# Kernel optimization log

Hardware: AMD Instinct MI355X
Metric: run time of the kernel (lower is better)

## Reference

```python
import jax, jax.numpy as jnp
import numpy as np

EMBED_DIM = 1024


def setup_inputs() -> dict:
    key = jax.random.key(0)
    ks = jax.random.split(key, 9)
    B, S, D = 4, 4096, EMBED_DIM
    s = 1.0 / np.sqrt(D)
    inp = {"x": jax.random.normal(ks[0], (B, S, D), dtype=jnp.float32)}
    names = ["q", "k", "v", "out"]
    for i, n in enumerate(names):
        inp[f"w_{n}"] = jax.random.uniform(ks[1 + 2 * i], (D, D), jnp.float32, -s, s)
        inp[f"b_{n}"] = jax.random.uniform(ks[2 + 2 * i], (D,), jnp.float32, -s, s)
    return inp


def reference(x, w_q, b_q, w_k, b_k, w_v, b_v, w_out, b_out):
    D = x.shape[-1]
    scaling = 1.0 / jnp.sqrt(jnp.asarray(D, x.dtype))
    q = jnp.einsum("bsd,ed->bse", x, w_q) + b_q
    k = jnp.einsum("bsd,ed->bse", x, w_k) + b_k
    v = jnp.einsum("bsd,ed->bse", x, w_v) + b_v
    # full [B, S, S] attention matrix, as in the original module
    scores = jnp.einsum("bqd,bkd->bqk", q, k) * scaling
    attn = jax.nn.softmax(scores, axis=-1)
    out = jnp.einsum("bqk,bkd->bqd", attn, v)
    return jnp.einsum("bsd,ed->bse", out, w_out) + b_out
```

## Files before the change

### kernel.cpp

```cpp
#include <hip/hip_runtime.h>
#include <hip/hip_bf16.h>

typedef __hip_bfloat16 bf16;
typedef __bf16 bf16x8 __attribute__((ext_vector_type(8)));
typedef float f32x4 __attribute__((ext_vector_type(4)));

#define B_ 4
#define S_ 4096
#define D_ 1024
#define BS_ 16384
#define N3_ 3072

__device__ __forceinline__ void gld_lds16(const void* g, void* l) {
    __builtin_amdgcn_global_load_lds(
        (const __attribute__((address_space(1))) void*)g,
        (__attribute__((address_space(3))) void*)l, 16, 0, 0);
}

__device__ __forceinline__ void cast4_one(const float* __restrict__ in,
                                          bf16* __restrict__ out, int i) {
    float4 v = ((const float4*)in)[i];
    union { ushort4 u; bf16 h[4]; } cv;
    cv.h[0] = __float2bfloat16(v.x);
    cv.h[1] = __float2bfloat16(v.y);
    cv.h[2] = __float2bfloat16(v.z);
    cv.h[3] = __float2bfloat16(v.w);
    ((ushort4*)out)[i] = cv.u;
}

__global__ __launch_bounds__(256) void prologue(
    const float* __restrict__ x, const float* __restrict__ wq,
    const float* __restrict__ wk, const float* __restrict__ wv,
    const float* __restrict__ wo, const float* __restrict__ bq,
    const float* __restrict__ bk, const float* __restrict__ bv,
    bf16* __restrict__ xb, bf16* __restrict__ Wc, bf16* __restrict__ Wo,
    float* __restrict__ bc, float* __restrict__ ls) {
    const int blk = blockIdx.x, tid = threadIdx.x;
    if (blk < 16384) {
        cast4_one(x, xb, blk * 256 + tid);
    } else if (blk < 20480) {
        int w = (blk - 16384) >> 10;
        int i = ((blk - 16384) & 1023) * 256 + tid;
        const float* src = (w == 0) ? wq : (w == 1) ? wk : (w == 2) ? wv : wo;
        bf16* dst = (w == 3) ? Wo : Wc + (long)w * D_ * D_;
        cast4_one(src, dst, i);
    } else if (blk < 20544) {
        ls[(blk - 20480) * 256 + tid] = 0.f;
    } else {
        for (int i = tid; i < N3_; i += 256)
            bc[i] = (i < 1024) ? bq[i] : (i < 2048) ? bk[i - 1024] : bv[i - 2048];
    }
}

__global__ __launch_bounds__(256) void transpose_v(const bf16* __restrict__ QKV,
                                                   bf16* __restrict__ VT) {
    __shared__ bf16 t[32][33];
    const int b = blockIdx.z;
    const bf16* Vb = QKV + (long)b * S_ * N3_ + 2048;
    bf16* VTb = VT + (long)b * D_ * S_;
    const int s0 = blockIdx.x * 32, d0 = blockIdx.y * 32;
    const int r = threadIdx.x >> 5, c = threadIdx.x & 31;
#pragma unroll
    for (int i = 0; i < 4; i++)
        t[r + i * 8][c] = Vb[(long)(s0 + r + i * 8) * N3_ + d0 + c];
    __syncthreads();
#pragma unroll
    for (int i = 0; i < 4; i++)
        VTb[(long)(d0 + r + i * 8) * S_ + s0 + c] = t[c][r + i * 8];
}

template <int EPI, int BM>
__global__ __launch_bounds__(256, 2) void gemm_nt(
    const bf16* __restrict__ A, int lda, long sA,
    const bf16* __restrict__ B, int ldb, long sB,
    void* __restrict__ Cout, int ldc, long sC,
    int K, const float* __restrict__ bias,
    float* __restrict__ rowsum, int sL, float scale) {
    constexpr int MI = BM / 32;
    __shared__ __align__(16) bf16 As[BM * 64];
    __shared__ __align__(16) bf16 Bs[128 * 64];
    const int tid = threadIdx.x;
    const int lane = tid & 63;
    const int wave = tid >> 6;
    const int bz = blockIdx.z;
    const int m0 = blockIdx.x * BM, n0 = blockIdx.y * 128;
    A += (long)bz * sA;
    B += (long)bz * sB;
    rowsum += (long)bz * sL;

    const int wr = (wave >> 1) * (BM / 2);
    const int wc = (wave & 1) * 64;
    const int fm = lane & 15;
    const int q4 = lane >> 4;
    const int sw = fm & 7;
    const int rd0 = ((q4 ^ sw) << 3);
    const int rd1 = (((4 + q4) ^ sw) << 3);

    f32x4 zero = {0.f, 0.f, 0.f, 0.f};
    f32x4 acc[MI][4];
#pragma unroll
    for (int i = 0; i < MI; i++)
#pragma unroll
        for (int j = 0; j < 4; j++) acc[i][j] = zero;

    for (int k0 = 0; k0 < K; k0 += 64) {
#pragma unroll
        for (int t = 0; t < BM / 32; t++) {
            int c = tid + t * 256;
            int row = c >> 3;
            int q = (((c & 7) ^ (row & 7)) << 3);
            gld_lds16(A + (long)(m0 + row) * lda + k0 + q, As + c * 8);
        }
#pragma unroll
        for (int t = 0; t < 4; t++) {
            int c = tid + t * 256;
            int row = c >> 3;
            int q = (((c & 7) ^ (row & 7)) << 3);
            gld_lds16(B + (long)(n0 + row) * ldb + k0 + q, Bs + c * 8);
        }
        __syncthreads();
#pragma unroll
        for (int kh = 0; kh < 2; kh++) {
            const int rdo = kh ? rd1 : rd0;
            bf16x8 af[MI], bfr[4];
#pragma unroll
            for (int i = 0; i < MI; i++)
                af[i] = *(const bf16x8*)(As + (wr + i * 16 + fm) * 64 + rdo);
#pragma unroll
            for (int j = 0; j < 4; j++)
                bfr[j] = *(const bf16x8*)(Bs + (wc + j * 16 + fm) * 64 + rdo);
#pragma unroll
            for (int i = 0; i < MI; i++)
#pragma unroll
                for (int j = 0; j < 4; j++)
                    acc[i][j] = __builtin_amdgcn_mfma_f32_16x16x32_bf16(
                        af[i], bfr[j], acc[i][j], 0, 0, 0);
        }
        __syncthreads();
    }

#pragma unroll
    for (int i = 0; i < MI; i++)
#pragma unroll
        for (int r = 0; r < 4; r++) {
            const int grow = m0 + wr + q4 * 4 + i * 16 + r;
            if constexpr (EPI == 0) {
#pragma unroll
                for (int j = 0; j < 4; j++) {
                    int gcol = n0 + wc + j * 16 + fm;
                    ((bf16*)Cout)[(long)bz * sC + (long)grow * ldc + gcol] =
                        __float2bfloat16(acc[i][j][r] + bias[gcol]);
                }
            } else if constexpr (EPI == 1) {
                float s = 0.f;
#pragma unroll
                for (int j = 0; j < 4; j++) {
                    int gcol = n0 + wc + j * 16 + fm;
                    float v = __expf(acc[i][j][r] * scale);
                    bf16 hv = __float2bfloat16(v);
                    ((bf16*)Cout)[(long)bz * sC + (long)grow * ldc + gcol] = hv;
                    s += __bfloat162float(hv);
                }
                s += __shfl_xor(s, 1, 16);
                s += __shfl_xor(s, 2, 16);
                s += __shfl_xor(s, 4, 16);
                s += __shfl_xor(s, 8, 16);
                if (fm == 0) atomicAdd(rowsum + grow, s);
            } else if constexpr (EPI == 2) {
                float inv = 1.0f / rowsum[grow];
#pragma unroll
                for (int j = 0; j < 4; j++) {
                    int gcol = n0 + wc + j * 16 + fm;
                    ((bf16*)Cout)[(long)bz * sC + (long)grow * ldc + gcol] =
                        __float2bfloat16(acc[i][j][r] * inv);
                }
            } else {
#pragma unroll
                for (int j = 0; j < 4; j++) {
                    int gcol = n0 + wc + j * 16 + fm;
                    ((float*)Cout)[(long)bz * sC + (long)grow * ldc + gcol] =
                        acc[i][j][r] + bias[gcol];
                }
            }
        }
}

__device__ __forceinline__ void stage_half(const bf16* __restrict__ g, int ld,
                                           bf16* __restrict__ l, int tid) {
#pragma unroll
    for (int t = 0; t < 2; t++) {
        const int ch = tid + t * 512;
        const int row = ch >> 2;
        const int q = (ch ^ (row >> 1)) & 3;
        gld_lds16(g + (long)row * ld + (q << 3), l + ch * 8);
    }
    asm volatile("" ::: "memory");
}

__device__ __forceinline__ void ds_a4(bf16x8 (&d)[4], const bf16* __restrict__ base,
                                      int ro, int wr, int fm, int rdo) {
#pragma unroll
    for (int i = 0; i < 4; i++)
        d[i] = *(const bf16x8*)(base + (wr + ro + i * 16 + fm) * 32 + rdo);
}

__device__ __forceinline__ void ds_b4(bf16x8 (&d)[4], const bf16* __restrict__ base,
                                      int wc, int fm, int rdo) {
#pragma unroll
    for (int j = 0; j < 4; j++)
        d[j] = *(const bf16x8*)(base + (wc + j * 16 + fm) * 32 + rdo);
}

template <int IO>
__device__ __forceinline__ void mfma16(f32x4 (&acc)[8][4], const bf16x8 (&a)[4],
                                       const bf16x8 (&b)[4]) {
    __builtin_amdgcn_s_setprio(1);
#pragma unroll
    for (int i = 0; i < 4; i++)
#pragma unroll
        for (int j = 0; j < 4; j++)
            acc[IO + i][j] = __builtin_amdgcn_mfma_f32_16x16x32_bf16(
                a[i], b[j], acc[IO + i][j], 0, 0, 0);
    __builtin_amdgcn_s_setprio(0);
}

#define BAR() __builtin_amdgcn_s_barrier()
#define VM4() asm volatile("s_waitcnt vmcnt(4)" ::: "memory")
#define VM0() asm volatile("s_waitcnt vmcnt(0)" ::: "memory")

template <bool LAST>
__device__ __forceinline__ void ktile(
    f32x4 (&acc)[8][4],
    const bf16* __restrict__ Agl, int lda,
    const bf16* __restrict__ Bgl, int ldb, int kn,
    const bf16* __restrict__ cA0, const bf16* __restrict__ cB0,
    const bf16* __restrict__ cA1, const bf16* __restrict__ cB1,
    bf16* __restrict__ nA0, bf16* __restrict__ nB0,
    bf16* __restrict__ nA1, bf16* __restrict__ nB1,
    int tid, int wr, int wc, int fm, int rdo) {
    bf16x8 a[4], b[4];
    ds_a4(a, cA0, 0, wr, fm, rdo);
    ds_b4(b, cB0, wc, fm, rdo);
    if constexpr (!LAST) stage_half(Agl + kn, lda, nA0, tid);
    BAR();
    mfma16<0>(acc, a, b);
    BAR();
    ds_a4(a, cA0, 64, wr, fm, rdo);
    if constexpr (!LAST) stage_half(Bgl + kn, ldb, nB0, tid);
    BAR();
    mfma16<4>(acc, a, b);
    if constexpr (!LAST) VM4(); else VM0();
    BAR();
    ds_a4(a, cA1, 0, wr, fm, rdo);
    ds_b4(b, cB1, wc, fm, rdo);
    if constexpr (!LAST) stage_half(Agl + kn + 32, lda, nA1, tid);
    BAR();
    mfma16<0>(acc, a, b);
    BAR();
    ds_a4(a, cA1, 64, wr, fm, rdo);
    if constexpr (!LAST) stage_half(Bgl + kn + 32, ldb, nB1, tid);
    BAR();
    mfma16<4>(acc, a, b);
    if constexpr (!LAST) {
        VM4();
        BAR();
    }
}

template <int EPI>
__global__ __launch_bounds__(512, 2) void gemm8(
    const bf16* __restrict__ A, int lda, long sA,
    const bf16* __restrict__ B, int ldb, long sB,
    void* __restrict__ Cout, int ldc, long sC,
    int K, const float* __restrict__ bias,
    float* __restrict__ rowsum, int sL, float scale) {
    __shared__ __align__(16) bf16 A0h0[256 * 32], A0h1[256 * 32];
    __shared__ __align__(16) bf16 A1h0[256 * 32], A1h1[256 * 32];
    __shared__ __align__(16) bf16 B0h0[256 * 32], B0h1[256 * 32];
    __shared__ __align__(16) bf16 B1h0[256 * 32], B1h1[256 * 32];
    const int tid = threadIdx.x;
    const int lane = tid & 63;
    const int wave = tid >> 6;
    const int bz = blockIdx.z;
    const int m0 = blockIdx.x * 256, n0 = blockIdx.y * 256;
    A += (long)bz * sA + (long)m0 * lda;
    B += (long)bz * sB + (long)n0 * ldb;
    rowsum += (long)bz * sL;

    const int wm = wave >> 2, wn = wave & 3;
    const int wr = wm * 128, wc = wn * 64;
    const int fm = lane & 15, q4 = lane >> 4;
    const int rdo = ((q4 ^ ((fm >> 1) & 3)) << 3);

    f32x4 zero = {0.f, 0.f, 0.f, 0.f};
    f32x4 acc[8][4];
#pragma unroll
    for (int i = 0; i < 8; i++)
#pragma unroll
        for (int j = 0; j < 4; j++) acc[i][j] = zero;

    const int NT = K >> 6;
    stage_half(A, lda, A0h0, tid);
    stage_half(B, ldb, B0h0, tid);
    stage_half(A + 32, lda, A0h1, tid);
    stage_half(B + 32, ldb, B0h1, tid);
    VM4();
    BAR();

    int t = 0;
    for (; t + 2 < NT; t += 2) {
        ktile<false>(acc, A, lda, B, ldb, (t + 1) << 6,
                     A0h0, B0h0, A0h1, B0h1, A1h0, B1h0, A1h1, B1h1,
                     tid, wr, wc, fm, rdo);
        ktile<false>(acc, A, lda, B, ldb, (t + 2) << 6,
                     A1h0, B1h0, A1h1, B1h1, A0h0, B0h0, A0h1, B0h1,
                     tid, wr, wc, fm, rdo);
    }
    ktile<false>(acc, A, lda, B, ldb, (NT - 1) << 6,
                 A0h0, B0h0, A0h1, B0h1, A1h0, B1h0, A1h1, B1h1,
                 tid, wr, wc, fm, rdo);
    ktile<true>(acc, A, lda, B, ldb, 0,
                A1h0, B1h0, A1h1, B1h1, A0h0, B0h0, A0h1, B0h1,
                tid, wr, wc, fm, rdo);

#pragma unroll
    for (int mi = 0; mi < 8; mi++)
#pragma unroll
        for (int r = 0; r < 4; r++) {
            const int grow = m0 + wr + mi * 16 + q4 * 4 + r;
            if constexpr (EPI == 0) {
#pragma unroll
                for (int j = 0; j < 4; j++) {
                    int gcol = n0 + wc + j * 16 + fm;
                    ((bf16*)Cout)[(long)bz * sC + (long)grow * ldc + gcol] =
                        __float2bfloat16(acc[mi][j][r] + bias[gcol]);
                }
            } else if constexpr (EPI == 1) {
                float s = 0.f;
#pragma unroll
                for (int j = 0; j < 4; j++) {
                    int gcol = n0 + wc + j * 16 + fm;
                    float v = __expf(acc[mi][j][r] * scale);
                    bf16 hv = __float2bfloat16(v);
                    ((bf16*)Cout)[(long)bz * sC + (long)grow * ldc + gcol] = hv;
                    s += __bfloat162float(hv);
                }
                s += __shfl_xor(s, 1, 16);
                s += __shfl_xor(s, 2, 16);
                s += __shfl_xor(s, 4, 16);
                s += __shfl_xor(s, 8, 16);
                if (fm == 0) atomicAdd(rowsum + grow, s);
            } else if constexpr (EPI == 2) {
                float inv = 1.0f / rowsum[grow];
#pragma unroll
                for (int j = 0; j < 4; j++) {
                    int gcol = n0 + wc + j * 16 + fm;
                    ((bf16*)Cout)[(long)bz * sC + (long)grow * ldc + gcol] =
                        __float2bfloat16(acc[mi][j][r] * inv);
                }
            } else {
#pragma unroll
                for (int j = 0; j < 4; j++) {
                    int gcol = n0 + wc + j * 16 + fm;
                    ((float*)Cout)[(long)bz * sC + (long)grow * ldc + gcol] =
                        acc[mi][j][r] + bias[gcol];
                }
            }
        }
}

extern "C" void kernel_launch(void* const* d_in, const int* in_sizes, int n_in,
                              void* d_out, int out_size, void* d_ws, size_t ws_size,
                              hipStream_t stream) {
    const float* x  = (const float*)d_in[0];
    const float* wq = (const float*)d_in[1];
    const float* bq = (const float*)d_in[2];
    const float* wk = (const float*)d_in[3];
    const float* bk = (const float*)d_in[4];
    const float* wv = (const float*)d_in[5];
    const float* bv = (const float*)d_in[6];
    const float* wo = (const float*)d_in[7];
    const float* bo = (const float*)d_in[8];
    (void)in_sizes; (void)n_in; (void)out_size;

    char* p = (char*)d_ws;
    bf16* Wc  = (bf16*)p;  p += (long)N3_ * D_ * 2;
    bf16* Wo  = (bf16*)p;  p += (long)D_ * D_ * 2;
    float* bc = (float*)p; p += N3_ * 4;
    bf16* QKV = (bf16*)p;  p += (long)BS_ * N3_ * 2;
    float* ls = (float*)p; p += (long)BS_ * 4;

    bf16* xb = (bf16*)d_out;

    const size_t base = 109129728UL;
    int tier;
    bf16 *VT, *E;
    if (ws_size >= base + 134217728UL) {
        tier = 2;
        E  = (bf16*)p;
        VT = (bf16*)((char*)d_out + 33554432);
    } else if (ws_size >= base + 33554432UL) {
        tier = 1;
        VT = (bf16*)p;
        E  = (bf16*)d_out;
    } else {
        tier = 0;
        VT = (bf16*)((char*)d_out + 33554432);
        E  = (bf16*)d_out;
    }

    prologue<<<dim3(20545), 256, 0, stream>>>(x, wq, wk, wv, wo, bq, bk, bv,
                                              xb, Wc, Wo, bc, ls);

    gemm8<0><<<dim3(BS_ / 256, N3_ / 256, 1), 512, 0, stream>>>(
        xb, D_, 0, Wc, D_, 0, QKV, N3_, 0, D_, bc, ls, 0, 1.f);

    transpose_v<<<dim3(S_ / 32, D_ / 32, B_), 256, 0, stream>>>(QKV, VT);

    if (tier == 2) {
        gemm8<1><<<dim3(16, 16, 4), 512, 0, stream>>>(
            QKV, N3_, (long)S_ * N3_, QKV + 1024, N3_, (long)S_ * N3_,
            E, S_, (long)S_ * S_, D_, nullptr, ls, S_, 0.03125f);
        gemm8<2><<<dim3(16, 4, 4), 512, 0, stream>>>(
            E, S_, (long)S_ * S_, VT, S_, (long)D_ * S_,
            QKV, N3_, (long)S_ * N3_, S_, nullptr, ls, S_, 1.f);
    } else if (tier == 1) {
        for (int pr = 0; pr < 2; ++pr) {
            const long qoff = (long)(2 * pr) * S_ * N3_;
            gemm_nt<1, 128><<<dim3(32, 32, 2), 256, 0, stream>>>(
                QKV + qoff, N3_, (long)S_ * N3_,
                QKV + qoff + 1024, N3_, (long)S_ * N3_,
                E, S_, (long)S_ * S_, D_, nullptr, ls + 2 * pr * S_, S_, 0.03125f);
            gemm_nt<2, 128><<<dim3(32, 8, 2), 256, 0, stream>>>(
                E, S_, (long)S_ * S_,
                VT + (long)(2 * pr) * D_ * S_, S_, (long)D_ * S_,
                QKV + qoff, N3_, (long)S_ * N3_, S_, nullptr, ls + 2 * pr * S_, S_, 1.f);
        }
    } else {
        for (int b = 0; b < B_; ++b) {
            const long qoff = (long)b * S_ * N3_;
            gemm_nt<1, 128><<<dim3(32, 32, 1), 256, 0, stream>>>(
                QKV + qoff, N3_, 0, QKV + qoff + 1024, N3_, 0,
                E, S_, 0, D_, nullptr, ls + b * S_, 0, 0.03125f);
            gemm_nt<2, 64><<<dim3(64, 8, 1), 256, 0, stream>>>(
                E, S_, 0, VT + (long)b * D_ * S_, S_, 0,
                QKV + qoff, N3_, 0, S_, nullptr, ls + b * S_, 0, 1.f);
        }
    }

    gemm8<3><<<dim3(BS_ / 256, D_ / 256, 1), 512, 0, stream>>>(
        QKV, N3_, 0, Wo, D_, 0, d_out, D_, 0, D_, bo, ls, 0, 1.f);
}
```

Baseline: 635.3 us.

## Restructure GEMM k-tile into bulk LDS reads, prefetch, then MFMA block

Replaces the interleaved four-phase k-tile (barrier between each LDS read, stage and MFMA group) with one phase per tile. All LDS fragments for both halves are read into registers first, all four global-to-LDS prefetches are issued, and then all MFMAs run, with a single full vmcnt(0) wait and barrier at the end. Scheduling barriers pin this order. Dropping most barriers should cut sync overhead, at the cost of more fragment registers and no partial-wait overlap of loads with compute.

```diff
diff --git a/kernel.cpp b/kernel.cpp
--- a/kernel.cpp
+++ b/kernel.cpp
@@ -194,7 +194,6 @@
         const int q = (ch ^ (row >> 1)) & 3;
         gld_lds16(g + (long)row * ld + (q << 3), l + ch * 8);
     }
-    asm volatile("" ::: "memory");
 }
 
 __device__ __forceinline__ void ds_a4(bf16x8 (&d)[4], const bf16* __restrict__ base,
@@ -225,44 +224,42 @@
 }
 
 #define BAR() __builtin_amdgcn_s_barrier()
-#define VM4() asm volatile("s_waitcnt vmcnt(4)" ::: "memory")
 #define VM0() asm volatile("s_waitcnt vmcnt(0)" ::: "memory")
+#define SB0() __builtin_amdgcn_sched_barrier(0)
 
 template <bool LAST>
-__device__ __forceinline__ void ktile(
+__device__ __forceinline__ void ktile2(
     f32x4 (&acc)[8][4],
     const bf16* __restrict__ Agl, int lda,
     const bf16* __restrict__ Bgl, int ldb, int kn,
-    const bf16* __restrict__ cA0, const bf16* __restrict__ cB0,
-    const bf16* __restrict__ cA1, const bf16* __restrict__ cB1,
-    bf16* __restrict__ nA0, bf16* __restrict__ nB0,
-    bf16* __restrict__ nA1, bf16* __restrict__ nB1,
+    const bf16* __restrict__ cA0, const bf16* __restrict__ cA1,
+    const bf16* __restrict__ cB0, const bf16* __restrict__ cB1,
+    bf16* __restrict__ nA0, bf16* __restrict__ nA1,
+    bf16* __restrict__ nB0, bf16* __restrict__ nB1,
     int tid, int wr, int wc, int fm, int rdo) {
-    bf16x8 a[4], b[4];
-    ds_a4(a, cA0, 0, wr, fm, rdo);
-    ds_b4(b, cB0, wc, fm, rdo);
-    if constexpr (!LAST) stage_half(Agl + kn, lda, nA0, tid);
-    BAR();
-    mfma16<0>(acc, a, b);
-    BAR();
-    ds_a4(a, cA0, 64, wr, fm, rdo);
-    if constexpr (!LAST) stage_half(Bgl + kn, ldb, nB0, tid);
-    BAR();
-    mfma16<4>(acc, a, b);
-    if constexpr (!LAST) VM4(); else VM0();
-    BAR();
-    ds_a4(a, cA1, 0, wr, fm, rdo);
-    ds_b4(b, cB1, wc, fm, rdo);
-    if constexpr (!LAST) stage_half(Agl + kn + 32, lda, nA1, tid);
-    BAR();
-    mfma16<0>(acc, a, b);
-    BAR();
-    ds_a4(a, cA1, 64, wr, fm, rdo);
-    if constexpr (!LAST) stage_half(Bgl + kn + 32, ldb, nB1, tid);
-    BAR();
-    mfma16<4>(acc, a, b);
+    bf16x8 a0[4], a1[4], b0[4];
+    bf16x8 c0[4], c1[4], d0[4];
+    ds_a4(a0, cA0, 0, wr, fm, rdo);
+    ds_a4(a1, cA0, 64, wr, fm, rdo);
+    ds_b4(b0, cB0, wc, fm, rdo);
+    ds_a4(c0, cA1, 0, wr, fm, rdo);
+    ds_a4(c1, cA1, 64, wr, fm, rdo);
+    ds_b4(d0, cB1, wc, fm, rdo);
+    SB0();
     if constexpr (!LAST) {
-        VM4();
+        stage_half(Agl + kn, lda, nA0, tid);
+        stage_half(Agl + kn + 32, lda, nA1, tid);
+        stage_half(Bgl + kn, ldb, nB0, tid);
+        stage_half(Bgl + kn + 32, ldb, nB1, tid);
+    }
+    SB0();
+    mfma16<0>(acc, a0, b0);
+    mfma16<4>(acc, a1, b0);
+    mfma16<0>(acc, c0, d0);
+    mfma16<4>(acc, c1, d0);
+    if constexpr (!LAST) {
+        SB0();
+        VM0();
         BAR();
     }
 }
@@ -301,27 +298,27 @@
 
     const int NT = K >> 6;
     stage_half(A, lda, A0h0, tid);
+    stage_half(A + 32, lda, A0h1, tid);
     stage_half(B, ldb, B0h0, tid);
-    stage_half(A + 32, lda, A0h1, tid);
     stage_half(B + 32, ldb, B0h1, tid);
-    VM4();
+    VM0();
     BAR();
 
     int t = 0;
     for (; t + 2 < NT; t += 2) {
-        ktile<false>(acc, A, lda, B, ldb, (t + 1) << 6,
-                     A0h0, B0h0, A0h1, B0h1, A1h0, B1h0, A1h1, B1h1,
-                     tid, wr, wc, fm, rdo);
-        ktile<false>(acc, A, lda, B, ldb, (t + 2) << 6,
-                     A1h0, B1h0, A1h1, B1h1, A0h0, B0h0, A0h1, B0h1,
-                     tid, wr, wc, fm, rdo);
-    }
-    ktile<false>(acc, A, lda, B, ldb, (NT - 1) << 6,
-                 A0h0, B0h0, A0h1, B0h1, A1h0, B1h0, A1h1, B1h1,
+        ktile2<false>(acc, A, lda, B, ldb, (t + 1) << 6,
+                      A0h0, A0h1, B0h0, B0h1, A1h0, A1h1, B1h0, B1h1,
+                      tid, wr, wc, fm, rdo);
+        ktile2<false>(acc, A, lda, B, ldb, (t + 2) << 6,
+                      A1h0, A1h1, B1h0, B1h1, A0h0, A0h1, B0h0, B0h1,
+                      tid, wr, wc, fm, rdo);
+    }
+    ktile2<false>(acc, A, lda, B, ldb, (NT - 1) << 6,
+                  A0h0, A0h1, B0h0, B0h1, A1h0, A1h1, B1h0, B1h1,
+                  tid, wr, wc, fm, rdo);
+    ktile2<true>(acc, A, lda, B, ldb, 0,
+                 A1h0, A1h1, B1h0, B1h1, A0h0, A0h1, B0h0, B0h1,
                  tid, wr, wc, fm, rdo);
-    ktile<true>(acc, A, lda, B, ldb, 0,
-                A1h0, B1h0, A1h1, B1h1, A0h0, B0h0, A0h1, B0h1,
-                tid, wr, wc, fm, rdo);
 
 #pragma unroll
     for (int mi = 0; mi < 8; mi++)
```

Result: slower. 652.8 us (+2.8%).
